# Kernel optimization log

Hardware: AMD Instinct MI355X
Metric: run time of the kernel (lower is better)

## Reference

```python
import jax, jax.numpy as jnp
import numpy as np

N = 20000      # nodes per type
E = 320000     # edges per relation
F = 512        # raw feature dim
H = 4          # attention heads
C = 128        # hidden_channels per head
B = 64         # batch_size (num graphs)
HH = H * C
INNER = 64
NEG_SLOPE = 0.2


def _gatv2(x_src, x_dst, ei, Wl, Wr, att, b):
    """PyG GATv2Conv (concat=True, add_self_loops=True, neg_slope=0.2).
    x_src:[Ns,Fin] x_dst:[Nd,Fin'] ei:[2,E] Wl,Wr:[Fin,H*C] att:[H,C] b:[H*C].
    Returns [Nd, H*C]. Self-loop edges appended (inputs assumed loop-free)."""
    n_dst = x_dst.shape[0]
    loop = jnp.arange(min(x_src.shape[0], n_dst), dtype=ei.dtype)
    src = jnp.concatenate([ei[0], loop])
    dst = jnp.concatenate([ei[1], loop])
    xl = (x_src @ Wl).reshape(-1, H, C)   # source-side transform
    xr = (x_dst @ Wr).reshape(-1, H, C)   # target-side transform
    e = jax.nn.leaky_relu(xl[src] + xr[dst], NEG_SLOPE)   # [E',H,C]
    logit = jnp.einsum('ehc,hc->eh', e, att)               # [E',H]
    m = jax.ops.segment_max(logit, dst, num_segments=n_dst)
    m = jnp.where(jnp.isfinite(m), m, 0.0)
    p = jnp.exp(logit - m[dst])
    s = jax.ops.segment_sum(p, dst, num_segments=n_dst)
    alpha = p / jnp.maximum(s[dst], 1e-16)                 # per-dst softmax
    out = jax.ops.segment_sum(alpha[:, :, None] * xl[src], dst, num_segments=n_dst)
    return out.reshape(n_dst, HH) + b


def _layer(x_i, x_j, ei_ii, ei_jj, ei_ij, ei_ji, Wl, Wr, att, b):
    # relation order: 0:(x_i->x_i) 1:(x_j->x_j) 2:(x_i->x_j) 3:(x_j->x_i); HeteroConv aggr='sum'
    oi = _gatv2(x_i, x_i, ei_ii, Wl[0], Wr[0], att[0], b[0]) \
       + _gatv2(x_j, x_i, ei_ji, Wl[3], Wr[3], att[3], b[3])
    oj = _gatv2(x_j, x_j, ei_jj, Wl[1], Wr[1], att[1], b[1]) \
       + _gatv2(x_i, x_j, ei_ij, Wl[2], Wr[2], att[2], b[2])
    # head-sum + tanh: x.view(-1, heads, hidden).sum(1).tanh()
    oi = jnp.tanh(oi.reshape(-1, H, C).sum(axis=1))
    oj = jnp.tanh(oj.reshape(-1, H, C).sum(axis=1))
    return oi, oj


def setup_inputs() -> dict:
    key = jax.random.key(0)
    ks = jax.random.split(key, 24)
    inp = {
        'x_i': jax.random.normal(ks[0], (N, F), jnp.float32),
        'x_j': jax.random.normal(ks[1], (N, F), jnp.float32),
        'ei_ii': jax.random.randint(ks[2], (2, E), 0, N, jnp.int32),
        'ei_jj': jax.random.randint(ks[3], (2, E), 0, N, jnp.int32),
        'ei_ij': jax.random.randint(ks[4], (2, E), 0, N, jnp.int32),
        'ei_ji': jax.random.randint(ks[5], (2, E), 0, N, jnp.int32),
        'batch_i': jnp.sort(jax.random.randint(ks[6], (N,), 0, B, jnp.int32)),
        'batch_j': jnp.sort(jax.random.randint(ks[7], (N,), 0, B, jnp.int32)),
        'Wl0': jax.random.normal(ks[8], (4, F, HH), jnp.float32) / np.sqrt(F),
        'Wr0': jax.random.normal(ks[9], (4, F, HH), jnp.float32) / np.sqrt(F),
        'att0': jax.random.normal(ks[10], (4, H, C), jnp.float32) / np.sqrt(C),
        'b0': jnp.zeros((4, HH), jnp.float32),
        'Wl1': jax.random.normal(ks[11], (4, C, HH), jnp.float32) / np.sqrt(C),
        'Wr1': jax.random.normal(ks[12], (4, C, HH), jnp.float32) / np.sqrt(C),
        'att1': jax.random.normal(ks[13], (4, H, C), jnp.float32) / np.sqrt(C),
        'b1': jnp.zeros((4, HH), jnp.float32),
        'W_out': jax.random.normal(ks[14], (C, 1), jnp.float32) / np.sqrt(C),
        'b_out': jnp.zeros((1,), jnp.float32),
        'W_i': jax.random.normal(ks[15], (C, INNER), jnp.float32) / np.sqrt(C),
        'b_i': jnp.zeros((INNER,), jnp.float32),
        'W_j': jax.random.normal(ks[16], (C, INNER), jnp.float32) / np.sqrt(C),
        'b_j': jnp.zeros((INNER,), jnp.float32),
    }
    return inp


def reference(x_i, x_j, ei_ii, ei_jj, ei_ij, ei_ji, batch_i, batch_j,
              Wl0, Wr0, att0, b0, Wl1, Wr1, att1, b1,
              W_out, b_out, W_i, b_i, W_j, b_j):
    x_i, x_j = _layer(x_i, x_j, ei_ii, ei_jj, ei_ij, ei_ji, Wl0, Wr0, att0, b0)
    x_i, x_j = _layer(x_i, x_j, ei_ii, ei_jj, ei_ij, ei_ji, Wl1, Wr1, att1, b1)
    # global_add_pool per graph, then unsqueeze(1) + tanh
    p_i = jnp.tanh(jax.ops.segment_sum(x_i, batch_i, num_segments=B))[:, None, :]  # [B,1,C]
    p_j = jnp.tanh(jax.ops.segment_sum(x_j, batch_j, num_segments=B))[:, None, :]
    y_i = p_i @ W_i + b_i   # [B,1,INNER]
    y_j = p_j @ W_j + b_j
    x = (p_i + p_j)[:, 0, :]            # cat along dim=1 then sum(dim=1)
    logits = jax.nn.sigmoid(x @ W_out + b_out)   # [B,1]
    return (logits, y_i, y_j)
```

## Files before the change

kernel.cpp:

```cpp
#include <hip/hip_runtime.h>

#define NN      20000
#define EE      320000
#define ETOT    340000
#define FD      512
#define HH_     4
#define CD      128
#define HHD     512
#define BG      64
#define INNERD  64

typedef __attribute__((ext_vector_type(8))) short bf16x8;
typedef __attribute__((ext_vector_type(4))) float f32x4;

__device__ __forceinline__ float bf2f(unsigned v) { return __uint_as_float(v << 16); }
__device__ __forceinline__ unsigned short f2bf(float f) {
    unsigned u = __float_as_uint(f);
    unsigned r = 0x7fffu + ((u >> 16) & 1u);
    return (unsigned short)((u + r) >> 16);
}
__device__ __forceinline__ void load8bf(const unsigned short* p, float* f) {
    uint4 u = *reinterpret_cast<const uint4*>(p);
    f[0] = bf2f(u.x & 0xffffu); f[1] = bf2f(u.x >> 16);
    f[2] = bf2f(u.y & 0xffffu); f[3] = bf2f(u.y >> 16);
    f[4] = bf2f(u.z & 0xffffu); f[5] = bf2f(u.z >> 16);
    f[6] = bf2f(u.w & 0xffffu); f[7] = bf2f(u.w >> 16);
}
__device__ __forceinline__ void split_f32(float x, unsigned short& hi, unsigned short& lo) {
    unsigned u = __float_as_uint(x);
    hi = (unsigned short)(u >> 16);
    float r = x - bf2f(hi);
    lo = (unsigned short)(__float_as_uint(r) >> 16);
}
template <typename TA>
__device__ __forceinline__ void splitA(const TA* p, size_t i, unsigned short& hi, unsigned short& lo);
template <>
__device__ __forceinline__ void splitA<float>(const float* p, size_t i, unsigned short& hi, unsigned short& lo) {
    split_f32(p[i], hi, lo);
}
template <>
__device__ __forceinline__ void splitA<unsigned short>(const unsigned short* p, size_t i, unsigned short& hi, unsigned short& lo) {
    hi = p[i]; lo = 0;
}

__global__ __launch_bounds__(256) void csr_hist(const int* __restrict__ ei, int* __restrict__ cnt) {
    int e = blockIdx.x * blockDim.x + threadIdx.x;
    if (e < EE) atomicAdd(&cnt[ei[EE + e]], 1);
}

__global__ __launch_bounds__(1024) void csr_scan(const int* __restrict__ cnt,
                                                 int* __restrict__ rowptr,
                                                 int* __restrict__ cursor) {
    __shared__ int part[1024];
    int t = threadIdx.x;
    int base = t * 20;
    int s = 0;
    #pragma unroll
    for (int i = 0; i < 20; ++i) { int n = base + i; if (n < NN) s += cnt[n] + 1; }
    part[t] = s;
    __syncthreads();
    for (int off = 1; off < 1024; off <<= 1) {
        int v = (t >= off) ? part[t - off] : 0;
        __syncthreads();
        part[t] += v;
        __syncthreads();
    }
    int run = (t > 0) ? part[t - 1] : 0;
    #pragma unroll
    for (int i = 0; i < 20; ++i) {
        int n = base + i;
        if (n < NN) { rowptr[n] = run; cursor[n] = run; run += cnt[n] + 1; }
    }
    if (t == 1023) rowptr[NN] = run;
}

__global__ __launch_bounds__(256) void csr_scatter16(const int* __restrict__ ei,
                                                     int* __restrict__ cursor,
                                                     unsigned short* __restrict__ srcs) {
    int idx = blockIdx.x * blockDim.x + threadIdx.x;
    if (idx >= ETOT) return;
    int src, dst;
    if (idx < EE) { src = ei[idx]; dst = ei[EE + idx]; }
    else          { src = dst = idx - EE; }
    int pos = atomicAdd(&cursor[dst], 1);
    srcs[pos] = (unsigned short)src;
}

__global__ __launch_bounds__(256) void wsplit_t(const float* __restrict__ W,
                                                unsigned short* __restrict__ Whi,
                                                unsigned short* __restrict__ Wlo,
                                                int K)
{
    __shared__ float tile[64][65];
    const int nt = 512 / 64;
    const int kt = K / 64;
    int bid = blockIdx.x;
    int in = bid % nt; int ik = (bid / nt) % kt; int r = bid / (nt * kt);
    int t = threadIdx.x;
    const float* Wr_ = W + (size_t)r * K * 512;
    #pragma unroll
    for (int rep = 0; rep < 16; ++rep) {
        int idx = rep * 256 + t;
        int kk = idx >> 6, nn = idx & 63;
        tile[kk][nn] = Wr_[(size_t)(ik * 64 + kk) * 512 + in * 64 + nn];
    }
    __syncthreads();
    #pragma unroll
    for (int rep = 0; rep < 16; ++rep) {
        int idx = rep * 256 + t;
        int nn = idx >> 6, kk = idx & 63;
        unsigned short h, l; split_f32(tile[kk][nn], h, l);
        size_t o = ((size_t)r * 512 + in * 64 + nn) * K + ik * 64 + kk;
        Whi[o] = h; Wlo[o] = l;
    }
}

template <typename TA, bool A_EXACT>
__global__ __launch_bounds__(256, 3) void gemm_mfma_t(
    const TA* __restrict__ A0, const TA* __restrict__ A1,
    const unsigned short* __restrict__ B0h, const unsigned short* __restrict__ B0l,
    const unsigned short* __restrict__ B1h, const unsigned short* __restrict__ B1l,
    unsigned short* __restrict__ C0, unsigned short* __restrict__ C1,
    int M, int K, int N)
{
    const int gx = gridDim.x, gy = gridDim.y;
    const int nwg = gx * gy * (int)gridDim.z;
    int b = ((int)blockIdx.z * gy + blockIdx.y) * gx + blockIdx.x;
    int xcd = b & 7, q8 = nwg >> 3, r8 = nwg & 7;
    int work = (xcd < r8 ? xcd * (q8 + 1) : r8 * (q8 + 1) + (xcd - r8) * q8) + (b >> 3);
    int bx = work % gx; int t2 = work / gx; int by = t2 % gy; int bz = t2 / gy;

    const TA* A = bz ? A1 : A0;
    const unsigned short* Bhg = bz ? B1h : B0h;
    const unsigned short* Blg = bz ? B1l : B0l;
    unsigned short* C = bz ? C1 : C0;

    __shared__ unsigned short Ah[128][40];
    __shared__ unsigned short Al[A_EXACT ? 1 : 128][40];
    __shared__ unsigned short Bh[128][40];
    __shared__ unsigned short Bl[128][40];

    const int tid = threadIdx.x;
    const int wave = tid >> 6, lane = tid & 63;
    const int quad = lane >> 4, lrow = lane & 15;
    const int wr = (wave >> 1) * 64, wc = (wave & 1) * 64;
    const int tileM = by * 128, tileN = bx * 128;

    const int srow = tid >> 1;
    const int sks  = (tid & 1) * 16;
    const int sgm  = tileM + srow;

    f32x4 acc[4][4] = {};

    for (int k0 = 0; k0 < K; k0 += 32) {
        if constexpr (!A_EXACT) {
            bf16x8 ph[2] = {{}, {}}, pl[2] = {{}, {}};
            if (sgm < M) {
                const float* Ap = (const float*)A + (size_t)sgm * K + k0 + sks;
                #pragma unroll
                for (int s = 0; s < 2; ++s) {
                    float4 f0 = reinterpret_cast<const float4*>(Ap)[2 * s];
                    float4 f1 = reinterpret_cast<const float4*>(Ap)[2 * s + 1];
                    float xv[8] = {f0.x, f0.y, f0.z, f0.w, f1.x, f1.y, f1.z, f1.w};
                    #pragma unroll
                    for (int pp = 0; pp < 4; ++pp) {
                        unsigned u0 = __float_as_uint(xv[2 * pp]);
                        unsigned u1 = __float_as_uint(xv[2 * pp + 1]);
                        reinterpret_cast<unsigned*>(&ph[s])[pp] =
                            __builtin_amdgcn_perm(u1, u0, 0x07060302u);
                        float r0 = xv[2 * pp]     - __uint_as_float(u0 & 0xffff0000u);
                        float r1 = xv[2 * pp + 1] - __uint_as_float(u1 & 0xffff0000u);
                        reinterpret_cast<unsigned*>(&pl[s])[pp] =
                            __builtin_amdgcn_perm(__float_as_uint(r1), __float_as_uint(r0), 0x07060302u);
                    }
                }
            }
            *reinterpret_cast<bf16x8*>(&Ah[srow][sks])     = ph[0];
            *reinterpret_cast<bf16x8*>(&Ah[srow][sks + 8]) = ph[1];
            *reinterpret_cast<bf16x8*>(&Al[srow][sks])     = pl[0];
            *reinterpret_cast<bf16x8*>(&Al[srow][sks + 8]) = pl[1];
        } else {
            bf16x8 v0 = {}, v1 = {};
            if (sgm < M) {
                const unsigned short* Ap = (const unsigned short*)A + (size_t)sgm * K + k0 + sks;
                v0 = reinterpret_cast<const bf16x8*>(Ap)[0];
                v1 = reinterpret_cast<const bf16x8*>(Ap)[1];
            }
            *reinterpret_cast<bf16x8*>(&Ah[srow][sks])     = v0;
            *reinterpret_cast<bf16x8*>(&Ah[srow][sks + 8]) = v1;
        }
        {
            const unsigned short* Bp = Bhg + (size_t)(tileN + srow) * K + k0 + sks;
            const unsigned short* Bq = Blg + (size_t)(tileN + srow) * K + k0 + sks;
            bf16x8 h0 = reinterpret_cast<const bf16x8*>(Bp)[0];
            bf16x8 h1 = reinterpret_cast<const bf16x8*>(Bp)[1];
            bf16x8 l0 = reinterpret_cast<const bf16x8*>(Bq)[0];
            bf16x8 l1 = reinterpret_cast<const bf16x8*>(Bq)[1];
            *reinterpret_cast<bf16x8*>(&Bh[srow][sks])     = h0;
            *reinterpret_cast<bf16x8*>(&Bh[srow][sks + 8]) = h1;
            *reinterpret_cast<bf16x8*>(&Bl[srow][sks])     = l0;
            *reinterpret_cast<bf16x8*>(&Bl[srow][sks + 8]) = l1;
        }
        __syncthreads();
        bf16x8 ah[4], al[4], bh[4], bl[4];
        #pragma unroll
        for (int mi = 0; mi < 4; ++mi) {
            ah[mi] = *reinterpret_cast<const bf16x8*>(&Ah[wr + mi * 16 + lrow][quad * 8]);
            if constexpr (!A_EXACT)
                al[mi] = *reinterpret_cast<const bf16x8*>(&Al[wr + mi * 16 + lrow][quad * 8]);
        }
        #pragma unroll
        for (int ni = 0; ni < 4; ++ni) {
            bh[ni] = *reinterpret_cast<const bf16x8*>(&Bh[wc + ni * 16 + lrow][quad * 8]);
            bl[ni] = *reinterpret_cast<const bf16x8*>(&Bl[wc + ni * 16 + lrow][quad * 8]);
        }
        #pragma unroll
        for (int mi = 0; mi < 4; ++mi)
            #pragma unroll
            for (int ni = 0; ni < 4; ++ni) {
                acc[mi][ni] = __builtin_amdgcn_mfma_f32_16x16x32_bf16(
                    ah[mi], bh[ni], acc[mi][ni], 0, 0, 0);
                acc[mi][ni] = __builtin_amdgcn_mfma_f32_16x16x32_bf16(
                    ah[mi], bl[ni], acc[mi][ni], 0, 0, 0);
                if constexpr (!A_EXACT)
                    acc[mi][ni] = __builtin_amdgcn_mfma_f32_16x16x32_bf16(
                        al[mi], bh[ni], acc[mi][ni], 0, 0, 0);
            }
        __syncthreads();
    }
    #pragma unroll
    for (int mi = 0; mi < 4; ++mi) {
        #pragma unroll
        for (int ni = 0; ni < 4; ++ni) {
            int gcol = tileN + wc + ni * 16 + lrow;
            #pragma unroll
            for (int r = 0; r < 4; ++r) {
                int grow = tileM + wr + mi * 16 + quad * 4 + r;
                if (grow < M)
                    C[(size_t)grow * N + gcol] = f2bf(acc[mi][ni][r]);
            }
        }
    }
}

template <typename TA, bool A_EXACT>
__global__ __launch_bounds__(256) void gemm_mfma(
    const TA* __restrict__ A0, const TA* __restrict__ A1,
    const float* __restrict__ B0, const float* __restrict__ B1, int ldb,
    unsigned short* __restrict__ C0, unsigned short* __restrict__ C1,
    int M, int K, int N)
{
    const TA* A = blockIdx.z ? A1 : A0;
    const float* B = blockIdx.z ? B1 : B0;
    unsigned short* C = blockIdx.z ? C1 : C0;

    __shared__ unsigned short Ah[64][40];
    __shared__ unsigned short Al[64][40];
    __shared__ unsigned short Bh[64][40];
    __shared__ unsigned short Bl[64][40];
    const int tid = threadIdx.x;
    const int wave = tid >> 6, lane = tid & 63;
    const int quad = lane >> 4, lrow = lane & 15;
    const int tileM = blockIdx.y * 64, tileN = blockIdx.x * 64;
    const int wm = (wave >> 1) * 32, wn = (wave & 1) * 32;

    f32x4 acc[2][2] = {};

    const int am = tid >> 2;
    const int aks = (tid & 3) * 8;
    const int bn = tid & 63;
    const int bk0 = (tid >> 6) * 8;

    for (int k0 = 0; k0 < K; k0 += 32) {
        {
            int gm = tileM + am;
            bf16x8 ph = {}, pl = {};
            if (gm < M) {
                #pragma unroll
                for (int j = 0; j < 8; ++j) {
                    unsigned short h, l;
                    splitA(A, (size_t)gm * K + k0 + aks + j, h, l);
                    ph[j] = (short)h; pl[j] = (short)l;
                }
            }
            *reinterpret_cast<bf16x8*>(&Ah[am][aks]) = ph;
            if (!A_EXACT) *reinterpret_cast<bf16x8*>(&Al[am][aks]) = pl;
        }
        {
            bf16x8 ph, pl;
            #pragma unroll
            for (int j = 0; j < 8; ++j) {
                unsigned short h, l;
                split_f32(B[(size_t)(k0 + bk0 + j) * ldb + tileN + bn], h, l);
                ph[j] = (short)h; pl[j] = (short)l;
            }
            *reinterpret_cast<bf16x8*>(&Bh[bn][bk0]) = ph;
            *reinterpret_cast<bf16x8*>(&Bl[bn][bk0]) = pl;
        }
        __syncthreads();
        bf16x8 ah[2], al[2], bh[2], bl[2];
        #pragma unroll
        for (int mi = 0; mi < 2; ++mi) {
            ah[mi] = *reinterpret_cast<const bf16x8*>(&Ah[wm + mi * 16 + lrow][quad * 8]);
            if (!A_EXACT)
                al[mi] = *reinterpret_cast<const bf16x8*>(&Al[wm + mi * 16 + lrow][quad * 8]);
        }
        #pragma unroll
        for (int ni = 0; ni < 2; ++ni) {
            bh[ni] = *reinterpret_cast<const bf16x8*>(&Bh[wn + ni * 16 + lrow][quad * 8]);
            bl[ni] = *reinterpret_cast<const bf16x8*>(&Bl[wn + ni * 16 + lrow][quad * 8]);
        }
        #pragma unroll
        for (int mi = 0; mi < 2; ++mi)
            #pragma unroll
            for (int ni = 0; ni < 2; ++ni) {
                acc[mi][ni] = __builtin_amdgcn_mfma_f32_16x16x32_bf16(
                    ah[mi], bh[ni], acc[mi][ni], 0, 0, 0);
                acc[mi][ni] = __builtin_amdgcn_mfma_f32_16x16x32_bf16(
                    ah[mi], bl[ni], acc[mi][ni], 0, 0, 0);
                if (!A_EXACT)
                    acc[mi][ni] = __builtin_amdgcn_mfma_f32_16x16x32_bf16(
                        al[mi], bh[ni], acc[mi][ni], 0, 0, 0);
            }
        __syncthreads();
    }
    #pragma unroll
    for (int mi = 0; mi < 2; ++mi) {
        #pragma unroll
        for (int ni = 0; ni < 2; ++ni) {
            int gcol = tileN + wn + ni * 16 + lrow;
            #pragma unroll
            for (int r = 0; r < 4; ++r) {
                int grow = tileM + wm + mi * 16 + quad * 4 + r;
                if (grow < M)
                    C[(size_t)grow * N + gcol] = f2bf(acc[mi][ni][r]);
            }
        }
    }
}

__global__ __launch_bounds__(256) void fused_aggr1(
    const int* __restrict__ rowptr, const unsigned short* __restrict__ srcs,
    const unsigned short* __restrict__ xl, const unsigned short* __restrict__ xr,
    const float* __restrict__ att,
    float* __restrict__ acc, int add_in, int fin_mode,
    const float* __restrict__ bA, const float* __restrict__ bB,
    unsigned short* __restrict__ z,
    const int* __restrict__ batch, float* __restrict__ pool)
{
    int dst = (int)((blockIdx.x * (size_t)blockDim.x + threadIdx.x) >> 6);
    int lane = threadIdx.x & 63;
    if (dst >= NN) return;
    int beg = rowptr[dst], end = rowptr[dst + 1];

    unsigned ub = *reinterpret_cast<const unsigned*>(xr + (size_t)dst * CD + lane * 2);
    float br0 = bf2f(ub & 0xffffu), br1 = bf2f(ub >> 16);
    float ta0 = att[lane * 2], ta1 = att[lane * 2 + 1];

    float n0 = 0.f, n1 = 0.f, den = 0.f;
    for (int k = beg; k < end; ++k) {
        int src = srcs[k];
        unsigned ua = *reinterpret_cast<const unsigned*>(xl + (size_t)src * CD + lane * 2);
        float a0 = bf2f(ua & 0xffffu), a1 = bf2f(ua >> 16);
        float v0 = a0 + br0, v1 = a1 + br1;
        v0 = (v0 > 0.f) ? v0 : 0.2f * v0;
        v1 = (v1 > 0.f) ? v1 : 0.2f * v1;
        float d = v0 * ta0 + v1 * ta1;
        #pragma unroll
        for (int off = 1; off < 64; off <<= 1)
            d += __shfl_xor(d, off);
        float p = expf(d);
        n0 += p * a0; n1 += p * a1; den += p;
    }
    float o0 = n0 / den, o1 = n1 / den;
    size_t ai = (size_t)dst * CD + lane * 2;
    if (add_in) { o0 += acc[ai]; o1 += acc[ai + 1]; }
    if (fin_mode == 0) {
        acc[ai] = o0; acc[ai + 1] = o1;
    } else {
        int c0 = lane * 2;
        float bb0 = 0.f, bb1 = 0.f;
        #pragma unroll
        for (int h = 0; h < HH_; ++h) {
            bb0 += bA[h * CD + c0]     + bB[h * CD + c0];
            bb1 += bA[h * CD + c0 + 1] + bB[h * CD + c0 + 1];
        }
        o0 = tanhf(o0 + bb0);
        o1 = tanhf(o1 + bb1);
        if (fin_mode == 1) {
            z[ai] = f2bf(o0); z[ai + 1] = f2bf(o1);
        } else {
            int b = batch[dst];
            atomicAdd(&pool[(size_t)b * CD + c0],     o0);
            atomicAdd(&pool[(size_t)b * CD + c0 + 1], o1);
        }
    }
}

__global__ __launch_bounds__(256) void fused_aggr4(
    const int* __restrict__ rowptr, const unsigned short* __restrict__ srcs,
    const unsigned short* __restrict__ xl, const unsigned short* __restrict__ xr,
    const float* __restrict__ att,
    float* __restrict__ acc, int add_in, int fin_mode,
    const float* __restrict__ bA, const float* __restrict__ bB,
    unsigned short* __restrict__ z,
    const int* __restrict__ batch, float* __restrict__ pool)
{
    int dst = (int)((blockIdx.x * (size_t)blockDim.x + threadIdx.x) >> 6);
    int lane = threadIdx.x & 63;
    if (dst >= NN) return;
    int beg = rowptr[dst], end = rowptr[dst + 1];

    float br[8], ta[8];
    load8bf(xr + (size_t)dst * HHD + lane * 8, br);
    #pragma unroll
    for (int j = 0; j < 8; ++j) ta[j] = att[lane * 8 + j];

    float n[8] = {}; float den = 0.f;
    for (int k = beg; k < end; ++k) {
        int src = srcs[k];
        float a[8];
        load8bf(xl + (size_t)src * HHD + lane * 8, a);
        float d = 0.f;
        #pragma unroll
        for (int j = 0; j < 8; ++j) {
            float v = a[j] + br[j];
            v = (v > 0.f) ? v : 0.2f * v;
            d += v * ta[j];
        }
        d += __shfl_xor(d, 1);
        d += __shfl_xor(d, 2);
        d += __shfl_xor(d, 4);
        d += __shfl_xor(d, 8);
        float p = expf(d);
        den += p;
        #pragma unroll
        for (int j = 0; j < 8; ++j) n[j] += p * a[j];
    }
    float inv = 1.f / den;
    float o[8];
    #pragma unroll
    for (int j = 0; j < 8; ++j) {
        o[j] = n[j] * inv;
        o[j] += __shfl_xor(o[j], 16);
        o[j] += __shfl_xor(o[j], 32);
    }
    if (lane < 16) {
        size_t ai = (size_t)dst * CD + lane * 8;
        if (add_in) {
            #pragma unroll
            for (int j = 0; j < 8; ++j) o[j] += acc[ai + j];
        }
        if (fin_mode == 0) {
            #pragma unroll
            for (int j = 0; j < 8; ++j) acc[ai + j] = o[j];
        } else {
            int c0 = lane * 8;
            #pragma unroll
            for (int j = 0; j < 8; ++j) {
                float bb = 0.f;
                #pragma unroll
                for (int h = 0; h < HH_; ++h)
                    bb += bA[h * CD + c0 + j] + bB[h * CD + c0 + j];
                o[j] = tanhf(o[j] + bb);
            }
            if (fin_mode == 1) {
                #pragma unroll
                for (int j = 0; j < 8; ++j) z[ai + j] = f2bf(o[j]);
            } else {
                #pragma unroll
                for (int j = 0; j < 8; ++j) acc[ai + j] = o[j];
            }
        }
    }
}

__global__ __launch_bounds__(512) void pool_reduce(
    const float* __restrict__ acc, const int* __restrict__ batch,
    float* __restrict__ pool)
{
    int b = blockIdx.x;
    int t = threadIdx.x & (CD - 1);
    int q = threadIdx.x >> 7;
    int lo, hi;
    { int l = 0, r = NN; while (l < r) { int m = (l + r) >> 1; if (batch[m] < b) l = m + 1; else r = m; } lo = l; }
    { int l = lo, r = NN; while (l < r) { int m = (l + r) >> 1; if (batch[m] <= b) l = m + 1; else r = m; } hi = l; }
    float s = 0.f;
    for (int nrow = lo + q; nrow < hi; nrow += 4)
        s += acc[(size_t)nrow * CD + t];
    __shared__ float red[4][CD];
    red[q][t] = s;
    __syncthreads();
    if (q == 0)
        pool[(size_t)b * CD + t] = red[0][t] + red[1][t] + red[2][t] + red[3][t];
}

__global__ __launch_bounds__(128) void head_kernel(
    const float* __restrict__ pool_i, const float* __restrict__ pool_j,
    const float* __restrict__ W_out, const float* __restrict__ b_out,
    const float* __restrict__ W_i, const float* __restrict__ b_i,
    const float* __restrict__ W_j, const float* __restrict__ b_j,
    float* __restrict__ out)
{
    int b = blockIdx.x;
    int t = threadIdx.x;
    __shared__ float pi[CD], pj[CD];
    pi[t] = tanhf(pool_i[(size_t)b * CD + t]);
    pj[t] = tanhf(pool_j[(size_t)b * CD + t]);
    __syncthreads();
    if (t < INNERD) {
        float a = b_i[t];
        for (int c = 0; c < CD; ++c) a += pi[c] * W_i[c * INNERD + t];
        out[BG + (size_t)b * INNERD + t] = a;
    } else {
        int k = t - INNERD;
        float a = b_j[k];
        for (int c = 0; c < CD; ++c) a += pj[c] * W_j[c * INNERD + k];
        out[BG + BG * INNERD + (size_t)b * INNERD + k] = a;
    }
    if (t == 0) {
        float a = b_out[0];
        for (int c = 0; c < CD; ++c) a += (pi[c] + pj[c]) * W_out[c];
        out[b] = 1.f / (1.f + expf(-a));
    }
}

struct Ws {
    unsigned short *xl, *xr, *z_i, *z_j;
    float* acc;
    int *rowptr[4];
    unsigned short *srcs[4];
    int *cnt, *cursor;
    float *pool_i, *pool_j;
    unsigned short *wt0l_h, *wt0l_l, *wt0r_h, *wt0r_l;
    unsigned short *wt1l_h, *wt1l_l, *wt1r_h, *wt1r_l;
};

static void build_csr(const int* ei, int* rowptr, unsigned short* srcs,
                      int* cnt, int* cursor, hipStream_t stream) {
    hipMemsetAsync(cnt, 0, NN * sizeof(int), stream);
    csr_hist<<<(EE + 255) / 256, 256, 0, stream>>>(ei, cnt);
    csr_scan<<<1, 1024, 0, stream>>>(cnt, rowptr, cursor);
    csr_scatter16<<<(ETOT + 255) / 256, 256, 0, stream>>>(ei, cursor, srcs);
}

template <typename TA, bool A_EXACT>
static void run_group_fat_t(const TA* srcA[2], const TA* dstA[2],
                            const int* rp[2], const unsigned short* sr[2],
                            const int rids[2], int K,
                            const unsigned short* WTl_h, const unsigned short* WTl_l,
                            const unsigned short* WTr_h, const unsigned short* WTr_l,
                            const float* att, const float* bias, int fin_mode,
                            unsigned short* zout, const int* batch, float* pool,
                            const Ws& w, hipStream_t stream)
{
    dim3 gg(HHD / 128, (NN + 127) / 128, 2);
    const int ablocks = NN / 4;
    for (int q = 0; q < 2; ++q) {
        int r = rids[q];
        size_t off = (size_t)r * HHD * K;
        gemm_mfma_t<TA, A_EXACT><<<gg, 256, 0, stream>>>(
            srcA[q], dstA[q],
            WTl_h + off, WTl_l + off, WTr_h + off, WTr_l + off,
            w.xl, w.xr, NN, K, HHD);
        int fm = (q == 1) ? fin_mode : 0;
        fused_aggr4<<<ablocks, 256, 0, stream>>>(
            rp[q], sr[q], w.xl, w.xr,
            att + (size_t)r * HHD,
            w.acc, q > 0 ? 1 : 0, fm,
            bias + (size_t)rids[0] * HHD, bias + (size_t)rids[1] * HHD,
            zout, batch, pool);
    }
}

template <typename TA, bool A_EXACT>
static void run_group_fat(const TA* srcA[2], const TA* dstA[2],
                          const int* rp[2], const unsigned short* sr[2],
                          const int rids[2], int K,
                          const float* Wl, const float* Wr, const float* att,
                          const float* bias, int fin_mode,
                          unsigned short* zout, const int* batch, float* pool,
                          const Ws& w, hipStream_t stream)
{
    dim3 gg(HHD / 64, (NN + 63) / 64, 2);
    const int ablocks = NN / 4;
    for (int q = 0; q < 2; ++q) {
        int r = rids[q];
        gemm_mfma<TA, A_EXACT><<<gg, 256, 0, stream>>>(
            srcA[q], dstA[q],
            Wl + (size_t)r * K * HHD, Wr + (size_t)r * K * HHD, HHD,
            w.xl, w.xr, NN, K, HHD);
        int fm = (q == 1) ? fin_mode : 0;
        fused_aggr4<<<ablocks, 256, 0, stream>>>(
            rp[q], sr[q], w.xl, w.xr,
            att + (size_t)r * HHD,
            w.acc, q > 0 ? 1 : 0, fm,
            bias + (size_t)rids[0] * HHD, bias + (size_t)rids[1] * HHD,
            zout, batch, pool);
    }
}

template <typename TA, bool A_EXACT>
static void run_group_thin(const TA* srcA[2], const TA* dstA[2],
                           const int* eis[2], const int rids[2], int K,
                           const float* Wl, const float* Wr, const float* att,
                           const float* bias, int fin_mode,
                           unsigned short* zout, const int* batch, float* pool,
                           const Ws& w, hipStream_t stream)
{
    dim3 gg(2, (NN + 63) / 64, 2);
    const int ablocks = NN / 4;
    for (int q = 0; q < 2; ++q) {
        int r = rids[q];
        build_csr(eis[q], w.rowptr[0], w.srcs[0], w.cnt, w.cursor, stream);
        for (int h = 0; h < HH_; ++h) {
            const float* WlS = Wl + (size_t)r * K * HHD + h * CD;
            const float* WrS = Wr + (size_t)r * K * HHD + h * CD;
            gemm_mfma<TA, A_EXACT><<<gg, 256, 0, stream>>>(
                srcA[q], dstA[q], WlS, WrS, HHD, w.xl, w.xr, NN, K, CD);
            int pass = q * HH_ + h;
            int fm = (pass == 2 * HH_ - 1) ? fin_mode : 0;
            fused_aggr1<<<ablocks, 256, 0, stream>>>(
                w.rowptr[0], w.srcs[0], w.xl, w.xr,
                att + (size_t)r * HHD + h * CD,
                w.acc, pass > 0 ? 1 : 0, fm,
                bias + (size_t)rids[0] * HHD, bias + (size_t)rids[1] * HHD,
                zout, batch, pool);
        }
    }
}

extern "C" void kernel_launch(void* const* d_in, const int* in_sizes, int n_in,
                              void* d_out, int out_size, void* d_ws, size_t ws_size,
                              hipStream_t stream)
{
    const float* x_i   = (const float*)d_in[0];
    const float* x_j   = (const float*)d_in[1];
    const int* ei_ii   = (const int*)d_in[2];
    const int* ei_jj   = (const int*)d_in[3];
    const int* ei_ij   = (const int*)d_in[4];
    const int* ei_ji   = (const int*)d_in[5];
    const int* batch_i = (const int*)d_in[6];
    const int* batch_j = (const int*)d_in[7];
    const float* Wl0   = (const float*)d_in[8];
    const float* Wr0   = (const float*)d_in[9];
    const float* att0  = (const float*)d_in[10];
    const float* b0    = (const float*)d_in[11];
    const float* Wl1   = (const float*)d_in[12];
    const float* Wr1   = (const float*)d_in[13];
    const float* att1  = (const float*)d_in[14];
    const float* b1    = (const float*)d_in[15];
    const float* W_out = (const float*)d_in[16];
    const float* b_out = (const float*)d_in[17];
    const float* W_i   = (const float*)d_in[18];
    const float* b_i   = (const float*)d_in[19];
    const float* W_j   = (const float*)d_in[20];
    const float* b_j   = (const float*)d_in[21];
    float* out = (float*)d_out;

    const size_t FAT2_BYTES = (size_t)NN * HHD * 2 * 2 + (size_t)NN * CD * 4
                            + (size_t)NN * CD * 2 * 2 + 4 * (size_t)ETOT * 2
                            + 4 * (size_t)(NN + 4) * 4 + (size_t)NN * 4 * 2
                            + (size_t)BG * CD * 4 * 2;
    const size_t FAT1_BYTES = (size_t)NN * HHD * 2 * 2 + (size_t)NN * CD * 4
                            + (size_t)NN * CD * 2 * 2 + (size_t)ETOT * 2
                            + (size_t)(NN + 4) * 4 + (size_t)NN * 4 * 2
                            + (size_t)BG * CD * 4 * 2;
    const size_t WT0_ONE = (size_t)4 * 512 * 512 * 2;
    const size_t WT1_ONE = (size_t)4 * 512 * 128 * 2;
    const size_t WT_BYTES = 4 * WT0_ONE + 4 * WT1_ONE;

    const int ncsr = (ws_size >= FAT2_BYTES) ? 4 : 1;
    const bool fat = (ws_size >= FAT1_BYTES);
    const bool fat_t = (ws_size >= FAT2_BYTES + WT_BYTES);

    Ws w;
    char* p = (char*)d_ws;
    size_t xbytes = fat ? (size_t)NN * HHD * 2 : (size_t)NN * CD * 2;
    w.xl     = (unsigned short*)p; p += xbytes;
    w.xr     = (unsigned short*)p; p += xbytes;
    w.acc    = (float*)p;          p += (size_t)NN * CD * 4;
    w.z_i    = (unsigned short*)p; p += (size_t)NN * CD * 2;
    w.z_j    = (unsigned short*)p; p += (size_t)NN * CD * 2;
    for (int r = 0; r < 4; ++r) {
        int rr = (r < ncsr) ? r : 0;
        if (r < ncsr) {
            w.rowptr[r] = (int*)p;            p += (size_t)(NN + 4) * 4;
            w.srcs[r]   = (unsigned short*)p; p += (size_t)ETOT * 2;
        } else {
            w.rowptr[r] = w.rowptr[rr]; w.srcs[r] = w.srcs[rr];
        }
    }
    w.cnt    = (int*)p;            p += (size_t)NN * 4;
    w.cursor = (int*)p;            p += (size_t)NN * 4;
    w.pool_i = (float*)p;          p += (size_t)BG * CD * 4;
    w.pool_j = (float*)p;          p += (size_t)BG * CD * 4;
    if (fat_t) {
        w.wt0l_h = (unsigned short*)p; p += WT0_ONE;
        w.wt0l_l = (unsigned short*)p; p += WT0_ONE;
        w.wt0r_h = (unsigned short*)p; p += WT0_ONE;
        w.wt0r_l = (unsigned short*)p; p += WT0_ONE;
        w.wt1l_h = (unsigned short*)p; p += WT1_ONE;
        w.wt1l_l = (unsigned short*)p; p += WT1_ONE;
        w.wt1r_h = (unsigned short*)p; p += WT1_ONE;
        w.wt1r_l = (unsigned short*)p; p += WT1_ONE;
    }

    hipMemsetAsync(w.pool_i, 0, (size_t)BG * CD * sizeof(float), stream);
    hipMemsetAsync(w.pool_j, 0, (size_t)BG * CD * sizeof(float), stream);

    const int* eis_all[4] = { ei_ii, ei_jj, ei_ij, ei_ji };
    const float* srcA0_i[2] = { x_i, x_j };  const float* dstA0_i[2] = { x_i, x_i };
    const float* srcA0_j[2] = { x_j, x_i };  const float* dstA0_j[2] = { x_j, x_j };
    const int rids_i[2] = { 0, 3 };
    const int rids_j[2] = { 1, 2 };
    const unsigned short* srcA1_i[2] = { w.z_i, w.z_j };
    const unsigned short* dstA1_i[2] = { w.z_i, w.z_i };
    const unsigned short* srcA1_j[2] = { w.z_j, w.z_i };
    const unsigned short* dstA1_j[2] = { w.z_j, w.z_j };

    if (fat_t) {
        for (int r = 0; r < 4; ++r)
            build_csr(eis_all[r], w.rowptr[r], w.srcs[r], w.cnt, w.cursor, stream);
        wsplit_t<<<4 * (FD / 64) * 8, 256, 0, stream>>>(Wl0, w.wt0l_h, w.wt0l_l, FD);
        wsplit_t<<<4 * (FD / 64) * 8, 256, 0, stream>>>(Wr0, w.wt0r_h, w.wt0r_l, FD);
        wsplit_t<<<4 * (CD / 64) * 8, 256, 0, stream>>>(Wl1, w.wt1l_h, w.wt1l_l, CD);
        wsplit_t<<<4 * (CD / 64) * 8, 256, 0, stream>>>(Wr1, w.wt1r_h, w.wt1r_l, CD);

        const int* rp_i[2] = { w.rowptr[0], w.rowptr[3] };
        const unsigned short* sr_i[2] = { w.srcs[0], w.srcs[3] };
        const int* rp_j[2] = { w.rowptr[1], w.rowptr[2] };
        const unsigned short* sr_j[2] = { w.srcs[1], w.srcs[2] };
        run_group_fat_t<float, false>(srcA0_i, dstA0_i, rp_i, sr_i, rids_i, FD,
                                      w.wt0l_h, w.wt0l_l, w.wt0r_h, w.wt0r_l,
                                      att0, b0, 1, w.z_i, nullptr, nullptr, w, stream);
        run_group_fat_t<float, false>(srcA0_j, dstA0_j, rp_j, sr_j, rids_j, FD,
                                      w.wt0l_h, w.wt0l_l, w.wt0r_h, w.wt0r_l,
                                      att0, b0, 1, w.z_j, nullptr, nullptr, w, stream);
        run_group_fat_t<unsigned short, true>(srcA1_i, dstA1_i, rp_i, sr_i, rids_i, CD,
                                              w.wt1l_h, w.wt1l_l, w.wt1r_h, w.wt1r_l,
                                              att1, b1, 2, nullptr, batch_i, w.pool_i, w, stream);
        pool_reduce<<<BG, 512, 0, stream>>>(w.acc, batch_i, w.pool_i);
        run_group_fat_t<unsigned short, true>(srcA1_j, dstA1_j, rp_j, sr_j, rids_j, CD,
                                              w.wt1l_h, w.wt1l_l, w.wt1r_h, w.wt1r_l,
                                              att1, b1, 2, nullptr, batch_j, w.pool_j, w, stream);
        pool_reduce<<<BG, 512, 0, stream>>>(w.acc, batch_j, w.pool_j);
    } else if (fat) {
        if (ncsr == 4) {
            for (int r = 0; r < 4; ++r)
                build_csr(eis_all[r], w.rowptr[r], w.srcs[r], w.cnt, w.cursor, stream);
            const int* rp_i[2] = { w.rowptr[0], w.rowptr[3] };
            const unsigned short* sr_i[2] = { w.srcs[0], w.srcs[3] };
            const int* rp_j[2] = { w.rowptr[1], w.rowptr[2] };
            const unsigned short* sr_j[2] = { w.srcs[1], w.srcs[2] };
            run_group_fat<float, false>(srcA0_i, dstA0_i, rp_i, sr_i, rids_i, FD,
                                        Wl0, Wr0, att0, b0, 1, w.z_i, nullptr, nullptr, w, stream);
            run_group_fat<float, false>(srcA0_j, dstA0_j, rp_j, sr_j, rids_j, FD,
                                        Wl0, Wr0, att0, b0, 1, w.z_j, nullptr, nullptr, w, stream);
            run_group_fat<unsigned short, true>(srcA1_i, dstA1_i, rp_i, sr_i, rids_i, CD,
                                                Wl1, Wr1, att1, b1, 2, nullptr, batch_i, w.pool_i, w, stream);
            pool_reduce<<<BG, 512, 0, stream>>>(w.acc, batch_i, w.pool_i);
            run_group_fat<unsigned short, true>(srcA1_j, dstA1_j, rp_j, sr_j, rids_j, CD,
                                                Wl1, Wr1, att1, b1, 2, nullptr, batch_j, w.pool_j, w, stream);
            pool_reduce<<<BG, 512, 0, stream>>>(w.acc, batch_j, w.pool_j);
        } else {
            for (int pass = 0; pass < 4; ++pass) {
                const int* rids = (pass & 1) ? rids_j : rids_i;
                for (int q = 0; q < 2; ++q) {
                    int r = rids[q];
                    build_csr(eis_all[r], w.rowptr[0], w.srcs[0], w.cnt, w.cursor, stream);
                    dim3 gg(HHD / 64, (NN + 63) / 64, 2);
                    if (pass < 2) {
                        const float* sa = (pass == 0) ? srcA0_i[q] : srcA0_j[q];
                        const float* da = (pass == 0) ? dstA0_i[q] : dstA0_j[q];
                        gemm_mfma<float, false><<<gg, 256, 0, stream>>>(
                            sa, da, Wl0 + (size_t)r * FD * HHD, Wr0 + (size_t)r * FD * HHD,
                            HHD, w.xl, w.xr, NN, FD, HHD);
                        fused_aggr4<<<NN / 4, 256, 0, stream>>>(
                            w.rowptr[0], w.srcs[0], w.xl, w.xr, att0 + (size_t)r * HHD,
                            w.acc, q, (q == 1) ? 1 : 0,
                            b0 + (size_t)rids[0] * HHD, b0 + (size_t)rids[1] * HHD,
                            (pass == 0) ? w.z_i : w.z_j, nullptr, nullptr);
                    } else {
                        const unsigned short* sa = (pass == 2) ? srcA1_i[q] : srcA1_j[q];
                        const unsigned short* da = (pass == 2) ? dstA1_i[q] : dstA1_j[q];
                        gemm_mfma<unsigned short, true><<<gg, 256, 0, stream>>>(
                            sa, da, Wl1 + (size_t)r * CD * HHD, Wr1 + (size_t)r * CD * HHD,
                            HHD, w.xl, w.xr, NN, CD, HHD);
                        fused_aggr4<<<NN / 4, 256, 0, stream>>>(
                            w.rowptr[0], w.srcs[0], w.xl, w.xr, att1 + (size_t)r * HHD,
                            w.acc, q, (q == 1) ? 2 : 0,
                            b1 + (size_t)rids[0] * HHD, b1 + (size_t)rids[1] * HHD,
                            nullptr, (pass == 2) ? batch_i : batch_j,
                            (pass == 2) ? w.pool_i : w.pool_j);
                    }
                }
                if (pass == 2)
                    pool_reduce<<<BG, 512, 0, stream>>>(w.acc, batch_i, w.pool_i);
                else if (pass == 3)
                    pool_reduce<<<BG, 512, 0, stream>>>(w.acc, batch_j, w.pool_j);
            }
        }
    } else {
        const int* eis_i[2] = { ei_ii, ei_ji };
        const int* eis_j[2] = { ei_jj, ei_ij };
        run_group_thin<float, false>(srcA0_i, dstA0_i, eis_i, rids_i, FD, Wl0, Wr0, att0, b0,
                                     1, w.z_i, nullptr, nullptr, w, stream);
        run_group_thin<float, false>(srcA0_j, dstA0_j, eis_j, rids_j, FD, Wl0, Wr0, att0, b0,
                                     1, w.z_j, nullptr, nullptr, w, stream);
        run_group_thin<unsigned short, true>(srcA1_i, dstA1_i, eis_i, rids_i, CD, Wl1, Wr1, att1, b1,
                                             2, nullptr, batch_i, w.pool_i, w, stream);
        run_group_thin<unsigned short, true>(srcA1_j, dstA1_j, eis_j, rids_j, CD, Wl1, Wr1, att1, b1,
                                             2, nullptr, batch_j, w.pool_j, w, stream);
    }

    head_kernel<<<BG, 128, 0, stream>>>(w.pool_i, w.pool_j, W_out, b_out,
                                        W_i, b_i, W_j, b_j, out);
}
```

Before: 1.482 ms.

## Batch both relations' GEMMs into one launch and fuse dual-relation aggregation

Adds a four-way batched GEMM kernel so both relations' left and right projections run in a single launch, using extra workspace buffers for the second relation. A fused aggregation kernel computes both relations' attention aggregation per destination node and sums them in registers, which removes the intermediate accumulator round trip and an extra launch. The edge loop is also unrolled by two to overlap gathers. It needs more workspace and is only taken when the workspace is large enough.

Measured after the change: 1.441 ms. 2.8% less time.

```diff
diff --git a/kernel.cpp b/kernel.cpp
--- a/kernel.cpp
+++ b/kernel.cpp
@@ -116,25 +116,11 @@
 }
 
 template <typename TA, bool A_EXACT>
-__global__ __launch_bounds__(256, 3) void gemm_mfma_t(
-    const TA* __restrict__ A0, const TA* __restrict__ A1,
-    const unsigned short* __restrict__ B0h, const unsigned short* __restrict__ B0l,
-    const unsigned short* __restrict__ B1h, const unsigned short* __restrict__ B1l,
-    unsigned short* __restrict__ C0, unsigned short* __restrict__ C1,
-    int M, int K, int N)
-{
-    const int gx = gridDim.x, gy = gridDim.y;
-    const int nwg = gx * gy * (int)gridDim.z;
-    int b = ((int)blockIdx.z * gy + blockIdx.y) * gx + blockIdx.x;
-    int xcd = b & 7, q8 = nwg >> 3, r8 = nwg & 7;
-    int work = (xcd < r8 ? xcd * (q8 + 1) : r8 * (q8 + 1) + (xcd - r8) * q8) + (b >> 3);
-    int bx = work % gx; int t2 = work / gx; int by = t2 % gy; int bz = t2 / gy;
-
-    const TA* A = bz ? A1 : A0;
-    const unsigned short* Bhg = bz ? B1h : B0h;
-    const unsigned short* Blg = bz ? B1l : B0l;
-    unsigned short* C = bz ? C1 : C0;
-
+__device__ __forceinline__ void gemm_body(
+    const TA* __restrict__ A, const unsigned short* __restrict__ Bhg,
+    const unsigned short* __restrict__ Blg, unsigned short* __restrict__ C,
+    int bx, int by, int M, int K, int N)
+{
     __shared__ unsigned short Ah[128][40];
     __shared__ unsigned short Al[A_EXACT ? 1 : 128][40];
     __shared__ unsigned short Bh[128][40];
@@ -244,6 +230,54 @@
 }
 
 template <typename TA, bool A_EXACT>
+__global__ __launch_bounds__(256, 3) void gemm_mfma_t(
+    const TA* __restrict__ A0, const TA* __restrict__ A1,
+    const unsigned short* __restrict__ B0h, const unsigned short* __restrict__ B0l,
+    const unsigned short* __restrict__ B1h, const unsigned short* __restrict__ B1l,
+    unsigned short* __restrict__ C0, unsigned short* __restrict__ C1,
+    int M, int K, int N)
+{
+    const int gx = gridDim.x, gy = gridDim.y;
+    const int nwg = gx * gy * (int)gridDim.z;
+    int b = ((int)blockIdx.z * gy + blockIdx.y) * gx + blockIdx.x;
+    int xcd = b & 7, q8 = nwg >> 3, r8 = nwg & 7;
+    int work = (xcd < r8 ? xcd * (q8 + 1) : r8 * (q8 + 1) + (xcd - r8) * q8) + (b >> 3);
+    int bx = work % gx; int t2 = work / gx; int by = t2 % gy; int bz = t2 / gy;
+
+    const TA* A = bz ? A1 : A0;
+    const unsigned short* Bhg = bz ? B1h : B0h;
+    const unsigned short* Blg = bz ? B1l : B0l;
+    unsigned short* C = bz ? C1 : C0;
+    gemm_body<TA, A_EXACT>(A, Bhg, Blg, C, bx, by, M, K, N);
+}
+
+template <typename TA, bool A_EXACT>
+__global__ __launch_bounds__(256, 3) void gemm_mfma_t4(
+    const TA* __restrict__ A0, const TA* __restrict__ A1,
+    const TA* __restrict__ A2, const TA* __restrict__ A3,
+    const unsigned short* __restrict__ B0h, const unsigned short* __restrict__ B0l,
+    const unsigned short* __restrict__ B1h, const unsigned short* __restrict__ B1l,
+    const unsigned short* __restrict__ B2h, const unsigned short* __restrict__ B2l,
+    const unsigned short* __restrict__ B3h, const unsigned short* __restrict__ B3l,
+    unsigned short* __restrict__ C0, unsigned short* __restrict__ C1,
+    unsigned short* __restrict__ C2, unsigned short* __restrict__ C3,
+    int M, int K, int N)
+{
+    const int gx = gridDim.x, gy = gridDim.y;
+    const int nwg = gx * gy * (int)gridDim.z;
+    int b = ((int)blockIdx.z * gy + blockIdx.y) * gx + blockIdx.x;
+    int xcd = b & 7, q8 = nwg >> 3, r8 = nwg & 7;
+    int work = (xcd < r8 ? xcd * (q8 + 1) : r8 * (q8 + 1) + (xcd - r8) * q8) + (b >> 3);
+    int bx = work % gx; int t2 = work / gx; int by = t2 % gy; int bz = t2 / gy;
+
+    const TA* A = bz == 0 ? A0 : bz == 1 ? A1 : bz == 2 ? A2 : A3;
+    const unsigned short* Bhg = bz == 0 ? B0h : bz == 1 ? B1h : bz == 2 ? B2h : B3h;
+    const unsigned short* Blg = bz == 0 ? B0l : bz == 1 ? B1l : bz == 2 ? B2l : B3l;
+    unsigned short* C = bz == 0 ? C0 : bz == 1 ? C1 : bz == 2 ? C2 : C3;
+    gemm_body<TA, A_EXACT>(A, Bhg, Blg, C, bx, by, M, K, N);
+}
+
+template <typename TA, bool A_EXACT>
 __global__ __launch_bounds__(256) void gemm_mfma(
     const TA* __restrict__ A0, const TA* __restrict__ A1,
     const float* __restrict__ B0, const float* __restrict__ B1, int ldb,
@@ -397,6 +431,75 @@
     }
 }
 
+__device__ __forceinline__ void gat_rel(
+    const int* __restrict__ rp, const unsigned short* __restrict__ sr,
+    const unsigned short* __restrict__ xl, const unsigned short* __restrict__ xr,
+    const float* __restrict__ att, int dst, int lane, float* o)
+{
+    int beg = rp[dst], end = rp[dst + 1];
+    float br[8], ta[8];
+    load8bf(xr + (size_t)dst * HHD + lane * 8, br);
+    #pragma unroll
+    for (int j = 0; j < 8; ++j) ta[j] = att[lane * 8 + j];
+
+    float n[8] = {}; float den = 0.f;
+    int k = beg;
+    for (; k + 2 <= end; k += 2) {
+        int s0 = sr[k], s1 = sr[k + 1];
+        float a0[8], a1[8];
+        load8bf(xl + (size_t)s0 * HHD + lane * 8, a0);
+        load8bf(xl + (size_t)s1 * HHD + lane * 8, a1);
+        float d0 = 0.f, d1 = 0.f;
+        #pragma unroll
+        for (int j = 0; j < 8; ++j) {
+            float v0 = a0[j] + br[j];
+            v0 = (v0 > 0.f) ? v0 : 0.2f * v0;
+            d0 += v0 * ta[j];
+            float v1 = a1[j] + br[j];
+            v1 = (v1 > 0.f) ? v1 : 0.2f * v1;
+            d1 += v1 * ta[j];
+        }
+        d0 += __shfl_xor(d0, 1);  d1 += __shfl_xor(d1, 1);
+        d0 += __shfl_xor(d0, 2);  d1 += __shfl_xor(d1, 2);
+        d0 += __shfl_xor(d0, 4);  d1 += __shfl_xor(d1, 4);
+        d0 += __shfl_xor(d0, 8);  d1 += __shfl_xor(d1, 8);
+        float p0 = expf(d0), p1 = expf(d1);
+        den += p0;
+        #pragma unroll
+        for (int j = 0; j < 8; ++j) n[j] += p0 * a0[j];
+        den += p1;
+        #pragma unroll
+        for (int j = 0; j < 8; ++j) n[j] += p1 * a1[j];
+    }
+    if (k < end) {
+        int s0 = sr[k];
+        float a0[8];
+        load8bf(xl + (size_t)s0 * HHD + lane * 8, a0);
+        float d0 = 0.f;
+        #pragma unroll
+        for (int j = 0; j < 8; ++j) {
+            float v0 = a0[j] + br[j];
+            v0 = (v0 > 0.f) ? v0 : 0.2f * v0;
+            d0 += v0 * ta[j];
+        }
+        d0 += __shfl_xor(d0, 1);
+        d0 += __shfl_xor(d0, 2);
+        d0 += __shfl_xor(d0, 4);
+        d0 += __shfl_xor(d0, 8);
+        float p0 = expf(d0);
+        den += p0;
+        #pragma unroll
+        for (int j = 0; j < 8; ++j) n[j] += p0 * a0[j];
+    }
+    float inv = 1.f / den;
+    #pragma unroll
+    for (int j = 0; j < 8; ++j) {
+        o[j] = n[j] * inv;
+        o[j] += __shfl_xor(o[j], 16);
+        o[j] += __shfl_xor(o[j], 32);
+    }
+}
+
 __global__ __launch_bounds__(256) void fused_aggr4(
     const int* __restrict__ rowptr, const unsigned short* __restrict__ srcs,
     const unsigned short* __restrict__ xl, const unsigned short* __restrict__ xr,
@@ -409,42 +512,10 @@
     int dst = (int)((blockIdx.x * (size_t)blockDim.x + threadIdx.x) >> 6);
     int lane = threadIdx.x & 63;
     if (dst >= NN) return;
-    int beg = rowptr[dst], end = rowptr[dst + 1];
-
-    float br[8], ta[8];
-    load8bf(xr + (size_t)dst * HHD + lane * 8, br);
-    #pragma unroll
-    for (int j = 0; j < 8; ++j) ta[j] = att[lane * 8 + j];
-
-    float n[8] = {}; float den = 0.f;
-    for (int k = beg; k < end; ++k) {
-        int src = srcs[k];
-        float a[8];
-        load8bf(xl + (size_t)src * HHD + lane * 8, a);
-        float d = 0.f;
-        #pragma unroll
-        for (int j = 0; j < 8; ++j) {
-            float v = a[j] + br[j];
-            v = (v > 0.f) ? v : 0.2f * v;
-            d += v * ta[j];
-        }
-        d += __shfl_xor(d, 1);
-        d += __shfl_xor(d, 2);
-        d += __shfl_xor(d, 4);
-        d += __shfl_xor(d, 8);
-        float p = expf(d);
-        den += p;
-        #pragma unroll
-        for (int j = 0; j < 8; ++j) n[j] += p * a[j];
-    }
-    float inv = 1.f / den;
+
     float o[8];
-    #pragma unroll
-    for (int j = 0; j < 8; ++j) {
-        o[j] = n[j] * inv;
-        o[j] += __shfl_xor(o[j], 16);
-        o[j] += __shfl_xor(o[j], 32);
-    }
+    gat_rel(rowptr, srcs, xl, xr, att, dst, lane, o);
+
     if (lane < 16) {
         size_t ai = (size_t)dst * CD + lane * 8;
         if (add_in) {
@@ -471,6 +542,49 @@
                 #pragma unroll
                 for (int j = 0; j < 8; ++j) acc[ai + j] = o[j];
             }
+        }
+    }
+}
+
+__global__ __launch_bounds__(256) void fused_aggr4d(
+    const int* __restrict__ rp0, const unsigned short* __restrict__ sr0,
+    const unsigned short* __restrict__ xl0, const unsigned short* __restrict__ xr0,
+    const float* __restrict__ attA,
+    const int* __restrict__ rp1, const unsigned short* __restrict__ sr1,
+    const unsigned short* __restrict__ xl1, const unsigned short* __restrict__ xr1,
+    const float* __restrict__ attB,
+    float* __restrict__ acc, int fin_mode,
+    const float* __restrict__ bA, const float* __restrict__ bB,
+    unsigned short* __restrict__ z,
+    const int* __restrict__ batch, float* __restrict__ pool)
+{
+    int dst = (int)((blockIdx.x * (size_t)blockDim.x + threadIdx.x) >> 6);
+    int lane = threadIdx.x & 63;
+    if (dst >= NN) return;
+
+    float o0[8], o1[8];
+    gat_rel(rp0, sr0, xl0, xr0, attA, dst, lane, o0);
+    gat_rel(rp1, sr1, xl1, xr1, attB, dst, lane, o1);
+    #pragma unroll
+    for (int j = 0; j < 8; ++j) o1[j] += o0[j];
+
+    if (lane < 16) {
+        size_t ai = (size_t)dst * CD + lane * 8;
+        int c0 = lane * 8;
+        #pragma unroll
+        for (int j = 0; j < 8; ++j) {
+            float bb = 0.f;
+            #pragma unroll
+            for (int h = 0; h < HH_; ++h)
+                bb += bA[h * CD + c0 + j] + bB[h * CD + c0 + j];
+            o1[j] = tanhf(o1[j] + bb);
+        }
+        if (fin_mode == 1) {
+            #pragma unroll
+            for (int j = 0; j < 8; ++j) z[ai + j] = f2bf(o1[j]);
+        } else {
+            #pragma unroll
+            for (int j = 0; j < 8; ++j) acc[ai + j] = o1[j];
         }
     }
 }
@@ -526,7 +640,7 @@
 }
 
 struct Ws {
-    unsigned short *xl, *xr, *z_i, *z_j;
+    unsigned short *xl, *xr, *xl2, *xr2, *z_i, *z_j;
     float* acc;
     int *rowptr[4];
     unsigned short *srcs[4];
@@ -542,6 +656,32 @@
     csr_hist<<<(EE + 255) / 256, 256, 0, stream>>>(ei, cnt);
     csr_scan<<<1, 1024, 0, stream>>>(cnt, rowptr, cursor);
     csr_scatter16<<<(ETOT + 255) / 256, 256, 0, stream>>>(ei, cursor, srcs);
+}
+
+template <typename TA, bool A_EXACT>
+static void run_group_fat_m(const TA* srcA[2], const TA* dstA[2],
+                            const int* rp[2], const unsigned short* sr[2],
+                            const int rids[2], int K,
+                            const unsigned short* WTl_h, const unsigned short* WTl_l,
+                            const unsigned short* WTr_h, const unsigned short* WTr_l,
+                            const float* att, const float* bias, int fin_mode,
+                            unsigned short* zout, const int* batch, float* pool,
+                            const Ws& w, hipStream_t stream)
+{
+    dim3 gg(HHD / 128, (NN + 127) / 128, 4);
+    size_t off0 = (size_t)rids[0] * HHD * K;
+    size_t off1 = (size_t)rids[1] * HHD * K;
+    gemm_mfma_t4<TA, A_EXACT><<<gg, 256, 0, stream>>>(
+        srcA[0], dstA[0], srcA[1], dstA[1],
+        WTl_h + off0, WTl_l + off0, WTr_h + off0, WTr_l + off0,
+        WTl_h + off1, WTl_l + off1, WTr_h + off1, WTr_l + off1,
+        w.xl, w.xr, w.xl2, w.xr2, NN, K, HHD);
+    fused_aggr4d<<<NN / 4, 256, 0, stream>>>(
+        rp[0], sr[0], w.xl, w.xr, att + (size_t)rids[0] * HHD,
+        rp[1], sr[1], w.xl2, w.xr2, att + (size_t)rids[1] * HHD,
+        w.acc, fin_mode,
+        bias + (size_t)rids[0] * HHD, bias + (size_t)rids[1] * HHD,
+        zout, batch, pool);
 }
 
 template <typename TA, bool A_EXACT>
@@ -669,10 +809,12 @@
     const size_t WT0_ONE = (size_t)4 * 512 * 512 * 2;
     const size_t WT1_ONE = (size_t)4 * 512 * 128 * 2;
     const size_t WT_BYTES = 4 * WT0_ONE + 4 * WT1_ONE;
+    const size_t X2_BYTES = 2 * (size_t)NN * HHD * 2;
 
     const int ncsr = (ws_size >= FAT2_BYTES) ? 4 : 1;
     const bool fat = (ws_size >= FAT1_BYTES);
     const bool fat_t = (ws_size >= FAT2_BYTES + WT_BYTES);
+    const bool fat_m = (ws_size >= FAT2_BYTES + WT_BYTES + X2_BYTES);
 
     Ws w;
     char* p = (char*)d_ws;
@@ -705,6 +847,10 @@
         w.wt1r_h = (unsigned short*)p; p += WT1_ONE;
         w.wt1r_l = (unsigned short*)p; p += WT1_ONE;
     }
+    if (fat_m) {
+        w.xl2 = (unsigned short*)p; p += (size_t)NN * HHD * 2;
+        w.xr2 = (unsigned short*)p; p += (size_t)NN * HHD * 2;
+    }
 
     hipMemsetAsync(w.pool_i, 0, (size_t)BG * CD * sizeof(float), stream);
     hipMemsetAsync(w.pool_j, 0, (size_t)BG * CD * sizeof(float), stream);
@@ -731,20 +877,38 @@
         const unsigned short* sr_i[2] = { w.srcs[0], w.srcs[3] };
         const int* rp_j[2] = { w.rowptr[1], w.rowptr[2] };
         const unsigned short* sr_j[2] = { w.srcs[1], w.srcs[2] };
-        run_group_fat_t<float, false>(srcA0_i, dstA0_i, rp_i, sr_i, rids_i, FD,
-                                      w.wt0l_h, w.wt0l_l, w.wt0r_h, w.wt0r_l,
-                                      att0, b0, 1, w.z_i, nullptr, nullptr, w, stream);
-        run_group_fat_t<float, false>(srcA0_j, dstA0_j, rp_j, sr_j, rids_j, FD,
-                                      w.wt0l_h, w.wt0l_l, w.wt0r_h, w.wt0r_l,
-                                      att0, b0, 1, w.z_j, nullptr, nullptr, w, stream);
-        run_group_fat_t<unsigned short, true>(srcA1_i, dstA1_i, rp_i, sr_i, rids_i, CD,
-                                              w.wt1l_h, w.wt1l_l, w.wt1r_h, w.wt1r_l,
-                                              att1, b1, 2, nullptr, batch_i, w.pool_i, w, stream);
-        pool_reduce<<<BG, 512, 0, stream>>>(w.acc, batch_i, w.pool_i);
-        run_group_fat_t<unsigned short, true>(srcA1_j, dstA1_j, rp_j, sr_j, rids_j, CD,
-                                              w.wt1l_h, w.wt1l_l, w.wt1r_h, w.wt1r_l,
-                                              att1, b1, 2, nullptr, batch_j, w.pool_j, w, stream);
-        pool_reduce<<<BG, 512, 0, stream>>>(w.acc, batch_j, w.pool_j);
+
+        if (fat_m) {
+            run_group_fat_m<float, false>(srcA0_i, dstA0_i, rp_i, sr_i, rids_i, FD,
+                                          w.wt0l_h, w.wt0l_l, w.wt0r_h, w.wt0r_l,
+                                          att0, b0, 1, w.z_i, nullptr, nullptr, w, stream);
+            run_group_fat_m<float, false>(srcA0_j, dstA0_j, rp_j, sr_j, rids_j, FD,
+                                          w.wt0l_h, w.wt0l_l, w.wt0r_h, w.wt0r_l,
+                                          att0, b0, 1, w.z_j, nullptr, nullptr, w, stream);
+            run_group_fat_m<unsigned short, true>(srcA1_i, dstA1_i, rp_i, sr_i, rids_i, CD,
+                                                  w.wt1l_h, w.wt1l_l, w.wt1r_h, w.wt1r_l,
+                                                  att1, b1, 2, nullptr, batch_i, w.pool_i, w, stream);
+            pool_reduce<<<BG, 512, 0, stream>>>(w.acc, batch_i, w.pool_i);
+            run_group_fat_m<unsigned short, true>(srcA1_j, dstA1_j, rp_j, sr_j, rids_j, CD,
+                                                  w.wt1l_h, w.wt1l_l, w.wt1r_h, w.wt1r_l,
+                                                  att1, b1, 2, nullptr, batch_j, w.pool_j, w, stream);
+            pool_reduce<<<BG, 512, 0, stream>>>(w.acc, batch_j, w.pool_j);
+        } else {
+            run_group_fat_t<float, false>(srcA0_i, dstA0_i, rp_i, sr_i, rids_i, FD,
+                                          w.wt0l_h, w.wt0l_l, w.wt0r_h, w.wt0r_l,
+                                          att0, b0, 1, w.z_i, nullptr, nullptr, w, stream);
+            run_group_fat_t<float, false>(srcA0_j, dstA0_j, rp_j, sr_j, rids_j, FD,
+                                          w.wt0l_h, w.wt0l_l, w.wt0r_h, w.wt0r_l,
+                                          att0, b0, 1, w.z_j, nullptr, nullptr, w, stream);
+            run_group_fat_t<unsigned short, true>(srcA1_i, dstA1_i, rp_i, sr_i, rids_i, CD,
+                                                  w.wt1l_h, w.wt1l_l, w.wt1r_h, w.wt1r_l,
+                                                  att1, b1, 2, nullptr, batch_i, w.pool_i, w, stream);
+            pool_reduce<<<BG, 512, 0, stream>>>(w.acc, batch_i, w.pool_i);
+            run_group_fat_t<unsigned short, true>(srcA1_j, dstA1_j, rp_j, sr_j, rids_j, CD,
+                                                  w.wt1l_h, w.wt1l_l, w.wt1r_h, w.wt1r_l,
+                                                  att1, b1, 2, nullptr, batch_j, w.pool_j, w, stream);
+            pool_reduce<<<BG, 512, 0, stream>>>(w.acc, batch_j, w.pool_j);
+        }
     } else if (fat) {
         if (ncsr == 4) {
             for (int r = 0; r < 4; ++r)
```
